# Kernel tuning notes

Hardware: AMD Instinct MI355X
Metric: run time of the kernel (lower is better)

Reference implementation:

```python
import jax, jax.numpy as jnp
import numpy as np

N = 50000      # nodes
E = 800000     # edges per relation
R = 2          # relations
L = 2          # conv layers
D = 128        # hidden / input channels
G = 64         # graphs in batch
C = 8          # num_classes


def setup_inputs() -> dict:
    key = jax.random.key(0)
    ks = jax.random.split(key, 6)
    x = jax.random.normal(ks[0], (N, D), dtype=jnp.float32)
    W = jax.random.normal(ks[1], (L, R, D, D), dtype=jnp.float32) * 0.05
    b = jnp.zeros((L, R, D), dtype=jnp.float32)
    lin_w = jax.random.normal(ks[2], (D, C), dtype=jnp.float32) * 0.05
    lin_b = jnp.zeros((C,), dtype=jnp.float32)
    edge_index = jax.random.randint(ks[3], (R, 2, E), 0, N, dtype=jnp.int32)
    batch = jnp.sort(jax.random.randint(ks[4], (N,), 0, G, dtype=jnp.int32))
    return {"x": x, "W": W, "b": b, "lin_w": lin_w, "lin_b": lin_b,
            "edge_index": edge_index, "batch": batch}


def _gcn_conv(x, src, dst, inv_sqrt_deg, W_r, b_r):
    """PyG GCNConv: symmetric-normalized aggregation with self loops.
    out[i] = sum_{j->i} d_i^-1/2 d_j^-1/2 (x_j W) + d_i^-1 (x_i W) + b
    where d includes the self loop (in-degree + 1)."""
    xw = x @ W_r                                   # [N, D]
    norm = inv_sqrt_deg[src] * inv_sqrt_deg[dst]   # [E]
    agg = jax.ops.segment_sum(xw[src] * norm[:, None], dst, num_segments=N)
    agg = agg + xw * (inv_sqrt_deg * inv_sqrt_deg)[:, None]  # self-loop msg
    return agg + b_r


def reference(x, W, b, lin_w, lin_b, edge_index, batch):
    # Pre-compute per-relation symmetric normalization (same for all layers).
    inv_sqrt_degs = []
    for r in range(R):
        dst = edge_index[r, 1]
        deg = jax.ops.segment_sum(jnp.ones((E,), x.dtype), dst, num_segments=N) + 1.0
        inv_sqrt_degs.append(jax.lax.rsqrt(deg))

    h = x
    for l in range(L):
        out = jnp.zeros((N, D), x.dtype)
        for r in range(R):  # HeteroConv aggr='sum' over relations
            out = out + _gcn_conv(h, edge_index[r, 0], edge_index[r, 1],
                                  inv_sqrt_degs[r], W[l, r], b[l, r])
        h = jax.nn.relu(out) if l < L - 1 else out

    # global_mean_pool over batch ids
    counts = jax.ops.segment_sum(jnp.ones((N,), x.dtype), batch, num_segments=G)
    sums = jax.ops.segment_sum(h, batch, num_segments=G)
    pooled = sums / jnp.maximum(counts, 1.0)[:, None]   # [G, D]
    # dropout(p=0.5) is identity in eval mode; final Linear
    return pooled @ lin_w + lin_b                        # [G, C]
```

## Files before the change

kernel.cpp:

```cpp
#include <hip/hip_runtime.h>
#include <math.h>

#define NN 50000
#define EE 800000
#define RR 2
#define LL 2
#define DD 128
#define GG 64
#define CCLS 8
#define NBUK 196
#define BCAP 6144
#define BCI  7424

typedef unsigned int uint;
typedef unsigned short ushort;
typedef short bf16x8 __attribute__((ext_vector_type(8)));
typedef float f32x4 __attribute__((ext_vector_type(4)));
typedef float f32x2 __attribute__((ext_vector_type(2)));

#define OFF_H1    ((size_t)0)
#define OFF_WBT   ((size_t)12800000)
#define OFF_ISD   ((size_t)12931072)
#define OFF_RP    ((size_t)13331072)
#define OFF_CI    ((size_t)14131072)
#define OFF_ZERO  ((size_t)25771904)
#define OFF_BD    ((size_t)25806592)
#define OFF_XW    ((size_t)25806592)
#define ZO_GCUR 0
#define ZO_SUM  1600
#define ZO_CNT  34368
#define ZERO_BYTES 34624

static __device__ __forceinline__ ushort f2b(float f) {
  uint u = __float_as_uint(f);
  uint r = (u + 0x7fffu + ((u >> 16) & 1u)) >> 16;
  return (ushort)r;
}
static __device__ __forceinline__ float blo(uint u) { return __uint_as_float(u << 16); }
static __device__ __forceinline__ float bhi(uint u) { return __uint_as_float(u & 0xffff0000u); }

__global__ __launch_bounds__(256) void k_wprep(const float* __restrict__ W,
                                               ushort* __restrict__ WT) {
  int idx = blockIdx.x * 256 + threadIdx.x;
  int lr = idx >> 14;
  int rem = idx & 16383;
  int n = rem >> 7, k = rem & 127;
  WT[lr * 16384 + n * 128 + k] = f2b(W[lr * 16384 + k * 128 + n]);
}

__global__ __launch_bounds__(256) void k_part(const int* __restrict__ EI,
                                              int* __restrict__ gcur,
                                              uint* __restrict__ bdata) {
  __shared__ int hist[256];
  __shared__ int sbase[256];
  __shared__ int gbase[256];
  __shared__ int lcur[256];
  __shared__ uint stage[4096];
  __shared__ unsigned char bstage[4096];
  const int r = blockIdx.y;
  const int t = threadIdx.x;
  const int e0 = blockIdx.x * 4096;
  const int cnt = min(4096, EE - e0);
  hist[t] = 0;
  lcur[t] = 0;
  __syncthreads();

  int src[16], dst[16];
  bool val[4];
#pragma unroll
  for (int j = 0; j < 4; ++j) {
    int i4 = (j * 256 + t) * 4;
    val[j] = (i4 < cnt);
    if (val[j]) {
      int4 s4 = *(const int4*)(EI + (size_t)r * 2 * EE + e0 + i4);
      int4 d4 = *(const int4*)(EI + (size_t)r * 2 * EE + EE + e0 + i4);
      src[j * 4 + 0] = s4.x; src[j * 4 + 1] = s4.y; src[j * 4 + 2] = s4.z; src[j * 4 + 3] = s4.w;
      dst[j * 4 + 0] = d4.x; dst[j * 4 + 1] = d4.y; dst[j * 4 + 2] = d4.z; dst[j * 4 + 3] = d4.w;
#pragma unroll
      for (int i = 0; i < 4; ++i) atomicAdd(&hist[dst[j * 4 + i] >> 8], 1);
    }
  }
  __syncthreads();
  int hv = hist[t];
  if (t < NBUK && hv > 0)
    gbase[t] = atomicAdd(&gcur[r * NBUK + t], hv);
  else
    gbase[t] = 0;
  sbase[t] = hv;
  __syncthreads();
  for (int off = 1; off < 256; off <<= 1) {
    int u = (t >= off) ? sbase[t - off] : 0;
    __syncthreads();
    sbase[t] += u;
    __syncthreads();
  }
  int incl = sbase[t];
  hist[t] = incl - hv;
  __syncthreads();
#pragma unroll
  for (int j = 0; j < 4; ++j) {
    if (val[j]) {
#pragma unroll
      for (int i = 0; i < 4; ++i) {
        int d = dst[j * 4 + i];
        int b = d >> 8;
        int p = atomicAdd(&lcur[b], 1);
        int pos = hist[b] + p;
        stage[pos] = ((uint)src[j * 4 + i] << 8) | (uint)(d & 255);
        bstage[pos] = (unsigned char)b;
      }
    }
  }
  __syncthreads();
  for (int s = t; s < cnt; s += 256) {
    int b = (int)bstage[s];
    bdata[(size_t)(r * NBUK + b) * BCAP + gbase[b] + (s - hist[b])] = stage[s];
  }
}

__global__ __launch_bounds__(256) void k_csr(const uint* __restrict__ bdata,
                                             const int* __restrict__ gcur,
                                             float* __restrict__ isd,
                                             int* __restrict__ rps,
                                             int* __restrict__ rpc,
                                             int* __restrict__ ci) {
  __shared__ int lcnt[256];
  __shared__ int lrp[256];
  __shared__ int lcur[256];
  __shared__ int cstage[BCI];
  __shared__ int shtot;
  const int b = blockIdx.x;
  const int r = blockIdx.y;
  const int t = threadIdx.x;
  const int cnt = gcur[r * NBUK + b];
  const uint* bd = bdata + (size_t)(r * NBUK + b) * BCAP;
  lcnt[t] = 0;
  lcur[t] = 0;
  __syncthreads();
  for (int s = t; s < cnt; s += 256) atomicAdd(&lcnt[bd[s] & 255u], 1);
  __syncthreads();
  const int deg = lcnt[t];
  const int node = b * 256 + t;
  const int valid = (node < NN) ? 1 : 0;
  const int deg3 = valid ? ((deg + 1 + 3) & ~3) : 0;
  lrp[t] = deg3;
  __syncthreads();
  for (int off = 1; off < 256; off <<= 1) {
    int u = (t >= off) ? lrp[t - off] : 0;
    __syncthreads();
    lrp[t] += u;
    __syncthreads();
  }
  int incl = lrp[t];
  if (t == 255) shtot = incl;
  __syncthreads();
  lrp[t] = incl - deg3;
  __syncthreads();
  const int ex = lrp[t];
  if (valid) {
    isd[r * NN + node] = rsqrtf((float)(deg + 1));
    rps[r * NN + node] = b * BCI + ex;
    rpc[r * NN + node] = deg3;
    cstage[ex + deg] = node;
    for (int p = deg + 1; p < deg3; ++p) cstage[ex + p] = NN;
  }
  const int btot = shtot;
  if (t < 16) cstage[btot + t] = NN;
  __syncthreads();
  for (int s = t; s < cnt; s += 256) {
    uint pr = bd[s];
    int j = (int)(pr & 255u);
    int p = atomicAdd(&lcur[j], 1);
    cstage[lrp[j] + p] = (int)(pr >> 8);
  }
  __syncthreads();
  const int on = btot + 16;
  int* co = ci + (size_t)r * (NBUK * BCI) + (size_t)b * BCI;
  for (int s = t; s < on; s += 256) co[s] = cstage[s];
}

#define AL_S 72
#define WT_S 136
template <int IN_BF16>
__global__ __launch_bounds__(256) void k_gemm(const void* __restrict__ Xv,
                                              const ushort* __restrict__ WTg,
                                              const float* __restrict__ isd,
                                              uint* __restrict__ Y) {
  __shared__ ushort WTl[128 * WT_S];
  __shared__ ushort Al[128 * AL_S];
  const int r = blockIdx.y;
  const int m0b = blockIdx.x * 128;
  const int t = threadIdx.x;
  const int w = t >> 6, L = t & 63, q = L >> 4, ln = L & 15;
  uint* Yr = Y + (size_t)r * (NN + 1) * 32;
  const ushort* WTr = WTg + (size_t)r * 16384;

#pragma unroll
  for (int i = 0; i < 8; ++i) {
    int g = t + i * 256;
    int n = g >> 4, k0 = (g & 15) * 8;
    *(uint4*)(&WTl[n * WT_S + k0]) = *(const uint4*)(WTr + n * 128 + k0);
  }

  f32x4 acc[2][8];
#pragma unroll
  for (int mt = 0; mt < 2; ++mt)
#pragma unroll
    for (int nt = 0; nt < 8; ++nt) {
      acc[mt][nt][0] = 0.f; acc[mt][nt][1] = 0.f;
      acc[mt][nt][2] = 0.f; acc[mt][nt][3] = 0.f;
    }

  for (int hh = 0; hh < 2; ++hh) {
    __syncthreads();
    {
      int row = t >> 1, ch = t & 1;
      int gm = m0b + row;
      ushort* dst = &Al[row * AL_S + ch * 32];
      if (gm < NN) {
        if (IN_BF16) {
          const uint4* xp = (const uint4*)((const ushort*)Xv + (size_t)gm * 128 + hh * 64 + ch * 32);
#pragma unroll
          for (int j = 0; j < 4; ++j) ((uint4*)dst)[j] = xp[j];
        } else {
          const float4* xp = (const float4*)((const float*)Xv + (size_t)gm * 128 + hh * 64 + ch * 32);
          ushort tmp[32];
#pragma unroll
          for (int j = 0; j < 8; ++j) {
            float4 v = xp[j];
            tmp[j * 4 + 0] = f2b(v.x); tmp[j * 4 + 1] = f2b(v.y);
            tmp[j * 4 + 2] = f2b(v.z); tmp[j * 4 + 3] = f2b(v.w);
          }
#pragma unroll
          for (int j = 0; j < 4; ++j) ((uint4*)dst)[j] = ((uint4*)tmp)[j];
        }
      } else {
        uint4 z = make_uint4(0, 0, 0, 0);
#pragma unroll
        for (int j = 0; j < 4; ++j) ((uint4*)dst)[j] = z;
      }
    }
    __syncthreads();
#pragma unroll
    for (int kk = 0; kk < 2; ++kk) {
      bf16x8 b0 = *(const bf16x8*)(&Al[(w * 32 + ln) * AL_S + kk * 32 + q * 8]);
      bf16x8 b1 = *(const bf16x8*)(&Al[(w * 32 + 16 + ln) * AL_S + kk * 32 + q * 8]);
#pragma unroll
      for (int nt = 0; nt < 8; ++nt) {
        bf16x8 a = *(const bf16x8*)(&WTl[(nt * 16 + ln) * WT_S + hh * 64 + kk * 32 + q * 8]);
        acc[0][nt] = __builtin_amdgcn_mfma_f32_16x16x32_bf16(a, b0, acc[0][nt], 0, 0, 0);
        acc[1][nt] = __builtin_amdgcn_mfma_f32_16x16x32_bf16(a, b1, acc[1][nt], 0, 0, 0);
      }
    }
  }
#pragma unroll
  for (int mt = 0; mt < 2; ++mt) {
    int m = m0b + w * 32 + mt * 16 + ln;
    if (m <= NN) {
      float sc = (m < NN) ? isd[r * NN + m] : 0.f;
      uint* yp = Yr + (size_t)m * 32;
#pragma unroll
      for (int nt = 0; nt < 8; ++nt) {
        f32x4 v = acc[mt][nt];
        uint u = __builtin_amdgcn_cvt_pk_fp8_f32(v[0] * sc, v[1] * sc, 0u, false);
        u = __builtin_amdgcn_cvt_pk_fp8_f32(v[2] * sc, v[3] * sc, u, true);
        yp[nt * 4 + q] = u;
      }
    }
  }
}

__global__ __launch_bounds__(256) void k_agg(const char* __restrict__ xw,
                                             const int* __restrict__ rps,
                                             const int* __restrict__ rpc,
                                             const int* __restrict__ ci,
                                             const float* __restrict__ isd,
                                             const float* __restrict__ bias,
                                             uint* __restrict__ hout, int relu_flag) {
  const int w = threadIdx.x >> 6;
  const int lane = threadIdx.x & 63;
  const int g = lane >> 4, c = lane & 15;
  const int i = blockIdx.x * 4 + w;
  const uint cb = (uint)c * 8u;

  f32x2 tot[4];
#pragma unroll
  for (int j = 0; j < 4; ++j) { tot[j][0] = 0.f; tot[j][1] = 0.f; }

#pragma unroll
  for (int r = 0; r < RR; ++r) {
    const char* xwr = xw + (size_t)r * ((size_t)(NN + 1) * 128);
    const int e0 = rps[r * NN + i];
    const int total = rpc[r * NN + i];
    const int* ce = ci + (size_t)r * (NBUK * BCI) + e0;
    const float di = isd[r * NN + i];

    f32x2 acc[4];
#pragma unroll
    for (int j = 0; j < 4; ++j) { acc[j][0] = 0.f; acc[j][1] = 0.f; }

    int s0 = ce[g];
    uint2 ucur = *(const uint2*)(xwr + (((uint)s0 << 7) + cb));
    int s1 = ce[4 + g];
    int ip = 8 + g;
    for (int base = 0; base < total; base += 4) {
      uint2 unext = *(const uint2*)(xwr + (((uint)s1 << 7) + cb));
      int s2 = ce[ip];
      ip += 4;
      f32x2 v;
      v = __builtin_amdgcn_cvt_pk_f32_fp8(ucur.x, false); acc[0] += v;
      v = __builtin_amdgcn_cvt_pk_f32_fp8(ucur.x, true);  acc[1] += v;
      v = __builtin_amdgcn_cvt_pk_f32_fp8(ucur.y, false); acc[2] += v;
      v = __builtin_amdgcn_cvt_pk_f32_fp8(ucur.y, true);  acc[3] += v;
      ucur = unext;
      s1 = s2;
    }
    f32x2 d2; d2[0] = di; d2[1] = di;
#pragma unroll
    for (int j = 0; j < 4; ++j) tot[j] += acc[j] * d2;
  }

#pragma unroll
  for (int mask = 16; mask <= 32; mask <<= 1) {
#pragma unroll
    for (int j = 0; j < 4; ++j) {
      f32x2 o;
      o[0] = __shfl_xor(tot[j][0], mask);
      o[1] = __shfl_xor(tot[j][1], mask);
      tot[j] += o;
    }
  }

  if (g == 0) {
    const int ch0 = c * 8;
    const float4* b0p = (const float4*)(bias + ch0);
    const float4* b1p = (const float4*)(bias + DD + ch0);
    float4 ba = b0p[0], bb = b0p[1], bc = b1p[0], bd = b1p[1];
    float o[8] = {tot[0][0], tot[0][1], tot[1][0], tot[1][1],
                  tot[2][0], tot[2][1], tot[3][0], tot[3][1]};
    o[0] += ba.x + bc.x; o[1] += ba.y + bc.y; o[2] += ba.z + bc.z; o[3] += ba.w + bc.w;
    o[4] += bb.x + bd.x; o[5] += bb.y + bd.y; o[6] += bb.z + bd.z; o[7] += bb.w + bd.w;
    if (relu_flag) {
#pragma unroll
      for (int j = 0; j < 8; ++j) o[j] = fmaxf(o[j], 0.f);
    }
    uint4 pk;
    pk.x = (uint)f2b(o[0]) | ((uint)f2b(o[1]) << 16);
    pk.y = (uint)f2b(o[2]) | ((uint)f2b(o[3]) << 16);
    pk.z = (uint)f2b(o[4]) | ((uint)f2b(o[5]) << 16);
    pk.w = (uint)f2b(o[6]) | ((uint)f2b(o[7]) << 16);
    ((uint4*)(hout + (size_t)i * 64))[c] = pk;
  }
}

#define PCHUNK 32
__global__ __launch_bounds__(64) void k_pool(const uint* __restrict__ h,
                                             const int* __restrict__ batch,
                                             float* __restrict__ sums,
                                             int* __restrict__ counts) {
  int lane = threadIdx.x;
  int n0 = blockIdx.x * PCHUNK;
  int n1 = n0 + PCHUNK;
  if (n1 > NN) n1 = NN;
  if (n0 >= NN) return;
  float aLo = 0.f, aHi = 0.f;
  int cnt = 0;
  int g = batch[n0];
  uint u = h[(size_t)n0 * 64 + lane];
  for (int n = n0; n < n1; ++n) {
    uint unext = 0;
    int gnext = g;
    if (n + 1 < n1) {
      unext = h[(size_t)(n + 1) * 64 + lane];
      gnext = batch[n + 1];
    }
    aLo += blo(u);
    aHi += bhi(u);
    cnt++;
    if (n + 1 < n1 && gnext != g) {
      atomicAdd(&sums[g * DD + lane * 2], aLo);
      atomicAdd(&sums[g * DD + lane * 2 + 1], aHi);
      if (lane == 0) atomicAdd(&counts[g], cnt);
      aLo = 0.f; aHi = 0.f; cnt = 0;
      g = gnext;
    }
    u = unext;
  }
  atomicAdd(&sums[g * DD + lane * 2], aLo);
  atomicAdd(&sums[g * DD + lane * 2 + 1], aHi);
  if (lane == 0) atomicAdd(&counts[g], cnt);
}

__global__ __launch_bounds__(512) void k_final(const float* __restrict__ sums,
                                               const int* __restrict__ counts,
                                               const float* __restrict__ lin_w,
                                               const float* __restrict__ lin_b,
                                               float* __restrict__ out) {
  int t = threadIdx.x;
  int g = t >> 3, co = t & 7;
  float cnt = (float)counts[g];
  if (cnt < 1.f) cnt = 1.f;
  float inv = 1.f / cnt;
  float v = lin_b[co];
  for (int d = 0; d < DD; ++d) v += (sums[g * DD + d] * inv) * lin_w[d * CCLS + co];
  out[t] = v;
}

extern "C" void kernel_launch(void* const* d_in, const int* in_sizes, int n_in,
                              void* d_out, int out_size, void* d_ws, size_t ws_size,
                              hipStream_t stream) {
  (void)in_sizes; (void)n_in; (void)out_size; (void)ws_size;
  const float* x     = (const float*)d_in[0];
  const float* W     = (const float*)d_in[1];
  const float* b     = (const float*)d_in[2];
  const float* lin_w = (const float*)d_in[3];
  const float* lin_b = (const float*)d_in[4];
  const int*   EI    = (const int*)d_in[5];
  const int*   batch = (const int*)d_in[6];
  float* out = (float*)d_out;

  char* ws = (char*)d_ws;
  uint*   h1    = (uint*)(ws + OFF_H1);
  ushort* WbfT  = (ushort*)(ws + OFF_WBT);
  float*  isd   = (float*)(ws + OFF_ISD);
  int*    rps   = (int*)(ws + OFF_RP);
  int*    rpc   = rps + 2 * NN;
  int*    ci    = (int*)(ws + OFF_CI);
  uint*   bdata = (uint*)(ws + OFF_BD);
  uint*   xw    = (uint*)(ws + OFF_XW);
  char*   zb    = ws + OFF_ZERO;
  int*    gcur  = (int*)(zb + ZO_GCUR);
  float*  sums  = (float*)(zb + ZO_SUM);
  int*    counts= (int*)(zb + ZO_CNT);

  (void)hipMemsetAsync(zb, 0, ZERO_BYTES, stream);

  k_wprep<<<256, 256, 0, stream>>>(W, WbfT);
  k_part<<<dim3((EE + 4095) / 4096, RR), 256, 0, stream>>>(EI, gcur, bdata);
  k_csr<<<dim3(NBUK, RR), 256, 0, stream>>>(bdata, gcur, isd, rps, rpc, ci);

  for (int l = 0; l < LL; ++l) {
    const ushort* WTl_g = WbfT + (size_t)l * RR * DD * DD;
    if (l == 0)
      k_gemm<0><<<dim3((NN + 127) / 128, RR), 256, 0, stream>>>((const void*)x, WTl_g, isd, xw);
    else
      k_gemm<1><<<dim3((NN + 127) / 128, RR), 256, 0, stream>>>((const void*)h1, WTl_g, isd, xw);
    k_agg<<<(NN + 3) / 4, 256, 0, stream>>>((const char*)xw, rps, rpc, ci, isd,
                                            b + (size_t)l * RR * DD, h1,
                                            (l < LL - 1) ? 1 : 0);
  }
  k_pool<<<(NN + PCHUNK - 1) / PCHUNK, 64, 0, stream>>>(h1, batch, sums, counts);
  k_final<<<1, GG * CCLS, 0, stream>>>(sums, counts, lin_w, lin_b, out);
}
```

Measured before the change: 289.3 us.

## Merge both relations into one CSR and process four nodes per wave in aggregation

The CSR build now runs one block per bucket for both relations together. It interleaves each node's neighbour lists for relation 0 and relation 1 into a single contiguous index stream, padded to groups of 8, with relation-1 indices offset into the second xw slab. The aggregation kernel assigns four consecutive nodes to each wave, uses 8 edge groups with 16-byte loads per lane, and keeps a continuous software pipeline across relations and nodes to hide gather latency and cut per-node setup. Padding to 8 adds wasted gathers for low-degree nodes, and the row-pointer layout and workspace offsets change.

```diff
diff --git a/kernel.cpp b/kernel.cpp
--- a/kernel.cpp
+++ b/kernel.cpp
@@ -10,7 +10,7 @@
 #define CCLS 8
 #define NBUK 196
 #define BCAP 6144
-#define BCI  7424
+#define BCI2 14080
 
 typedef unsigned int uint;
 typedef unsigned short ushort;
@@ -22,10 +22,10 @@
 #define OFF_WBT   ((size_t)12800000)
 #define OFF_ISD   ((size_t)12931072)
 #define OFF_RP    ((size_t)13331072)
-#define OFF_CI    ((size_t)14131072)
-#define OFF_ZERO  ((size_t)25771904)
-#define OFF_BD    ((size_t)25806592)
-#define OFF_XW    ((size_t)25806592)
+#define OFF_CI    ((size_t)13732480)
+#define OFF_ZERO  ((size_t)24771200)
+#define OFF_BD    ((size_t)24805824)
+#define OFF_XW    ((size_t)24805824)
 #define ZO_GCUR 0
 #define ZO_SUM  1600
 #define ZO_CNT  34368
@@ -124,26 +124,29 @@
                                              int* __restrict__ rps,
                                              int* __restrict__ rpc,
                                              int* __restrict__ ci) {
-  __shared__ int lcnt[256];
-  __shared__ int lrp[256];
-  __shared__ int lcur[256];
-  __shared__ int cstage[BCI];
+  __shared__ int lcnt0[256], lcnt1[256], lrp[256], lex[256], lng[256];
+  __shared__ int lcurA[256], lcurB[256];
+  __shared__ int cstage[BCI2];
   __shared__ int shtot;
   const int b = blockIdx.x;
-  const int r = blockIdx.y;
   const int t = threadIdx.x;
-  const int cnt = gcur[r * NBUK + b];
-  const uint* bd = bdata + (size_t)(r * NBUK + b) * BCAP;
-  lcnt[t] = 0;
-  lcur[t] = 0;
-  __syncthreads();
-  for (int s = t; s < cnt; s += 256) atomicAdd(&lcnt[bd[s] & 255u], 1);
-  __syncthreads();
-  const int deg = lcnt[t];
+  const int cnt0 = gcur[b];
+  const int cnt1 = gcur[NBUK + b];
+  const uint* bd0 = bdata + (size_t)b * BCAP;
+  const uint* bd1 = bdata + (size_t)(NBUK + b) * BCAP;
+  lcnt0[t] = 0; lcnt1[t] = 0; lcurA[t] = 0; lcurB[t] = 0;
+  __syncthreads();
+  for (int s = t; s < cnt0; s += 256) atomicAdd(&lcnt0[bd0[s] & 255u], 1);
+  for (int s = t; s < cnt1; s += 256) atomicAdd(&lcnt1[bd1[s] & 255u], 1);
+  __syncthreads();
+  const int deg0 = lcnt0[t];
+  const int deg1 = lcnt1[t];
   const int node = b * 256 + t;
   const int valid = (node < NN) ? 1 : 0;
-  const int deg3 = valid ? ((deg + 1 + 3) & ~3) : 0;
-  lrp[t] = deg3;
+  const int ng0 = valid ? ((deg0 + 8) >> 3) : 0;
+  const int ng1 = valid ? ((deg1 + 8) >> 3) : 0;
+  const int sz = (ng0 + ng1) << 3;
+  lrp[t] = sz;
   __syncthreads();
   for (int off = 1; off < 256; off <<= 1) {
     int u = (t >= off) ? lrp[t - off] : 0;
@@ -151,31 +154,40 @@
     lrp[t] += u;
     __syncthreads();
   }
-  int incl = lrp[t];
+  const int incl = lrp[t];
   if (t == 255) shtot = incl;
-  __syncthreads();
-  lrp[t] = incl - deg3;
-  __syncthreads();
-  const int ex = lrp[t];
+  const int ex = incl - sz;
+  lex[t] = ex;
+  lng[t] = ng0;
+  __syncthreads();
+  const int btot = shtot;
+  if (t < 32) cstage[btot + t] = NN;
+  rps[node] = b * BCI2 + ex;
+  rpc[node] = ng0 | (ng1 << 16);
   if (valid) {
-    isd[r * NN + node] = rsqrtf((float)(deg + 1));
-    rps[r * NN + node] = b * BCI + ex;
-    rpc[r * NN + node] = deg3;
-    cstage[ex + deg] = node;
-    for (int p = deg + 1; p < deg3; ++p) cstage[ex + p] = NN;
-  }
-  const int btot = shtot;
-  if (t < 16) cstage[btot + t] = NN;
-  __syncthreads();
-  for (int s = t; s < cnt; s += 256) {
-    uint pr = bd[s];
+    isd[node] = rsqrtf((float)(deg0 + 1));
+    isd[NN + node] = rsqrtf((float)(deg1 + 1));
+    cstage[ex + deg0] = node;
+    for (int p = deg0 + 1; p < (ng0 << 3); ++p) cstage[ex + p] = NN;
+    const int ex1 = ex + (ng0 << 3);
+    cstage[ex1 + deg1] = (NN + 1) + node;
+    for (int p = deg1 + 1; p < (ng1 << 3); ++p) cstage[ex1 + p] = NN;
+  }
+  for (int s = t; s < cnt0; s += 256) {
+    uint pr = bd0[s];
     int j = (int)(pr & 255u);
-    int p = atomicAdd(&lcur[j], 1);
-    cstage[lrp[j] + p] = (int)(pr >> 8);
-  }
-  __syncthreads();
-  const int on = btot + 16;
-  int* co = ci + (size_t)r * (NBUK * BCI) + (size_t)b * BCI;
+    int p = atomicAdd(&lcurA[j], 1);
+    cstage[lex[j] + p] = (int)(pr >> 8);
+  }
+  for (int s = t; s < cnt1; s += 256) {
+    uint pr = bd1[s];
+    int j = (int)(pr & 255u);
+    int p = atomicAdd(&lcurB[j], 1);
+    cstage[lex[j] + (lng[j] << 3) + p] = (int)(pr >> 8) + (NN + 1);
+  }
+  __syncthreads();
+  const int on = btot + 32;
+  int* co = ci + (size_t)b * BCI2;
   for (int s = t; s < on; s += 256) co[s] = cstage[s];
 }
 
@@ -270,6 +282,22 @@
   }
 }
 
+#define AGG_STEP()                                                           \
+  {                                                                          \
+    int s3 = ce0[ip]; ip += 8;                                               \
+    uint4 u2 = *(const uint4*)(xw + ((size_t)((uint)s2 << 7) + cb));         \
+    f32x2 v;                                                                 \
+    v = __builtin_amdgcn_cvt_pk_f32_fp8(u0.x, false); acc[0] += v;           \
+    v = __builtin_amdgcn_cvt_pk_f32_fp8(u0.x, true);  acc[1] += v;           \
+    v = __builtin_amdgcn_cvt_pk_f32_fp8(u0.y, false); acc[2] += v;           \
+    v = __builtin_amdgcn_cvt_pk_f32_fp8(u0.y, true);  acc[3] += v;           \
+    v = __builtin_amdgcn_cvt_pk_f32_fp8(u0.z, false); acc[4] += v;           \
+    v = __builtin_amdgcn_cvt_pk_f32_fp8(u0.z, true);  acc[5] += v;           \
+    v = __builtin_amdgcn_cvt_pk_f32_fp8(u0.w, false); acc[6] += v;           \
+    v = __builtin_amdgcn_cvt_pk_f32_fp8(u0.w, true);  acc[7] += v;           \
+    u0 = u1; u1 = u2; s2 = s3;                                               \
+  }
+
 __global__ __launch_bounds__(256) void k_agg(const char* __restrict__ xw,
                                              const int* __restrict__ rps,
                                              const int* __restrict__ rpc,
@@ -279,77 +307,82 @@
                                              uint* __restrict__ hout, int relu_flag) {
   const int w = threadIdx.x >> 6;
   const int lane = threadIdx.x & 63;
-  const int g = lane >> 4, c = lane & 15;
-  const int i = blockIdx.x * 4 + w;
-  const uint cb = (uint)c * 8u;
-
-  f32x2 tot[4];
-#pragma unroll
-  for (int j = 0; j < 4; ++j) { tot[j][0] = 0.f; tot[j][1] = 0.f; }
-
-#pragma unroll
-  for (int r = 0; r < RR; ++r) {
-    const char* xwr = xw + (size_t)r * ((size_t)(NN + 1) * 128);
-    const int e0 = rps[r * NN + i];
-    const int total = rpc[r * NN + i];
-    const int* ce = ci + (size_t)r * (NBUK * BCI) + e0;
-    const float di = isd[r * NN + i];
-
-    f32x2 acc[4];
-#pragma unroll
-    for (int j = 0; j < 4; ++j) { acc[j][0] = 0.f; acc[j][1] = 0.f; }
-
-    int s0 = ce[g];
-    uint2 ucur = *(const uint2*)(xwr + (((uint)s0 << 7) + cb));
-    int s1 = ce[4 + g];
-    int ip = 8 + g;
-    for (int base = 0; base < total; base += 4) {
-      uint2 unext = *(const uint2*)(xwr + (((uint)s1 << 7) + cb));
-      int s2 = ce[ip];
-      ip += 4;
-      f32x2 v;
-      v = __builtin_amdgcn_cvt_pk_f32_fp8(ucur.x, false); acc[0] += v;
-      v = __builtin_amdgcn_cvt_pk_f32_fp8(ucur.x, true);  acc[1] += v;
-      v = __builtin_amdgcn_cvt_pk_f32_fp8(ucur.y, false); acc[2] += v;
-      v = __builtin_amdgcn_cvt_pk_f32_fp8(ucur.y, true);  acc[3] += v;
-      ucur = unext;
-      s1 = s2;
-    }
-    f32x2 d2; d2[0] = di; d2[1] = di;
-#pragma unroll
-    for (int j = 0; j < 4; ++j) tot[j] += acc[j] * d2;
-  }
-
-#pragma unroll
-  for (int mask = 16; mask <= 32; mask <<= 1) {
-#pragma unroll
-    for (int j = 0; j < 4; ++j) {
-      f32x2 o;
-      o[0] = __shfl_xor(tot[j][0], mask);
-      o[1] = __shfl_xor(tot[j][1], mask);
-      tot[j] += o;
-    }
-  }
-
-  if (g == 0) {
-    const int ch0 = c * 8;
-    const float4* b0p = (const float4*)(bias + ch0);
-    const float4* b1p = (const float4*)(bias + DD + ch0);
-    float4 ba = b0p[0], bb = b0p[1], bc = b1p[0], bd = b1p[1];
-    float o[8] = {tot[0][0], tot[0][1], tot[1][0], tot[1][1],
-                  tot[2][0], tot[2][1], tot[3][0], tot[3][1]};
-    o[0] += ba.x + bc.x; o[1] += ba.y + bc.y; o[2] += ba.z + bc.z; o[3] += ba.w + bc.w;
-    o[4] += bb.x + bd.x; o[5] += bb.y + bd.y; o[6] += bb.z + bd.z; o[7] += bb.w + bd.w;
-    if (relu_flag) {
-#pragma unroll
-      for (int j = 0; j < 8; ++j) o[j] = fmaxf(o[j], 0.f);
-    }
-    uint4 pk;
-    pk.x = (uint)f2b(o[0]) | ((uint)f2b(o[1]) << 16);
-    pk.y = (uint)f2b(o[2]) | ((uint)f2b(o[3]) << 16);
-    pk.z = (uint)f2b(o[4]) | ((uint)f2b(o[5]) << 16);
-    pk.w = (uint)f2b(o[6]) | ((uint)f2b(o[7]) << 16);
-    ((uint4*)(hout + (size_t)i * 64))[c] = pk;
+  const int g = lane >> 3, c = lane & 7;
+  const int wid = blockIdx.x * 4 + w;
+  const int n0 = (wid >> 6) * 256 + (wid & 63) * 4;
+  const size_t cb = (size_t)c * 16;
+
+  const int m0 = rpc[n0], m1 = rpc[n0 + 1], m2 = rpc[n0 + 2], m3 = rpc[n0 + 3];
+  const int* ce0 = ci + rps[n0];
+
+  int ip = g;
+  int s0 = ce0[ip]; ip += 8;
+  int s1 = ce0[ip]; ip += 8;
+  int s2 = ce0[ip]; ip += 8;
+  uint4 u0 = *(const uint4*)(xw + ((size_t)((uint)s0 << 7) + cb));
+  uint4 u1 = *(const uint4*)(xw + ((size_t)((uint)s1 << 7) + cb));
+
+#pragma unroll
+  for (int k = 0; k < 4; ++k) {
+    const int node = n0 + k;
+    const int meta_k = (k == 0) ? m0 : (k == 1) ? m1 : (k == 2) ? m2 : m3;
+    const int ng0 = meta_k & 0xffff;
+    const int ng1 = (meta_k >> 16) & 0xffff;
+    const float di0 = isd[node];
+    const float di1 = isd[NN + node];
+
+    f32x2 acc[8];
+#pragma unroll
+    for (int j = 0; j < 8; ++j) { acc[j][0] = 0.f; acc[j][1] = 0.f; }
+    for (int q = 0; q < ng0; ++q) AGG_STEP();
+    f32x2 t8[8];
+    {
+      f32x2 d; d[0] = di0; d[1] = di0;
+#pragma unroll
+      for (int j = 0; j < 8; ++j) { t8[j] = acc[j] * d; acc[j][0] = 0.f; acc[j][1] = 0.f; }
+    }
+    for (int q = 0; q < ng1; ++q) AGG_STEP();
+    {
+      f32x2 d; d[0] = di1; d[1] = di1;
+#pragma unroll
+      for (int j = 0; j < 8; ++j) t8[j] += acc[j] * d;
+    }
+
+#pragma unroll
+    for (int mask = 8; mask <= 32; mask <<= 1) {
+#pragma unroll
+      for (int j = 0; j < 8; ++j) {
+        f32x2 o;
+        o[0] = __shfl_xor(t8[j][0], mask);
+        o[1] = __shfl_xor(t8[j][1], mask);
+        t8[j] += o;
+      }
+    }
+
+    if (g == 0 && node < NN) {
+      const float4* p0 = (const float4*)(bias + c * 16);
+      const float4* p1 = (const float4*)(bias + DD + c * 16);
+      float o[16];
+#pragma unroll
+      for (int j = 0; j < 4; ++j) {
+        float4 a = p0[j], bq = p1[j];
+        o[4 * j + 0] = t8[2 * j][0] + a.x + bq.x;
+        o[4 * j + 1] = t8[2 * j][1] + a.y + bq.y;
+        o[4 * j + 2] = t8[2 * j + 1][0] + a.z + bq.z;
+        o[4 * j + 3] = t8[2 * j + 1][1] + a.w + bq.w;
+      }
+      if (relu_flag) {
+#pragma unroll
+        for (int j = 0; j < 16; ++j) o[j] = fmaxf(o[j], 0.f);
+      }
+      uint pk[8];
+#pragma unroll
+      for (int j = 0; j < 8; ++j)
+        pk[j] = (uint)f2b(o[2 * j]) | ((uint)f2b(o[2 * j + 1]) << 16);
+      uint4* dst = (uint4*)(hout + (size_t)node * 64) + c * 2;
+      dst[0] = make_uint4(pk[0], pk[1], pk[2], pk[3]);
+      dst[1] = make_uint4(pk[4], pk[5], pk[6], pk[7]);
+    }
   }
 }
 
@@ -424,7 +457,7 @@
   ushort* WbfT  = (ushort*)(ws + OFF_WBT);
   float*  isd   = (float*)(ws + OFF_ISD);
   int*    rps   = (int*)(ws + OFF_RP);
-  int*    rpc   = rps + 2 * NN;
+  int*    rpc   = rps + NBUK * 256;
   int*    ci    = (int*)(ws + OFF_CI);
   uint*   bdata = (uint*)(ws + OFF_BD);
   uint*   xw    = (uint*)(ws + OFF_XW);
@@ -437,7 +470,7 @@
 
   k_wprep<<<256, 256, 0, stream>>>(W, WbfT);
   k_part<<<dim3((EE + 4095) / 4096, RR), 256, 0, stream>>>(EI, gcur, bdata);
-  k_csr<<<dim3(NBUK, RR), 256, 0, stream>>>(bdata, gcur, isd, rps, rpc, ci);
+  k_csr<<<NBUK, 256, 0, stream>>>(bdata, gcur, isd, rps, rpc, ci);
 
   for (int l = 0; l < LL; ++l) {
     const ushort* WTl_g = WbfT + (size_t)l * RR * DD * DD;
@@ -445,9 +478,9 @@
       k_gemm<0><<<dim3((NN + 127) / 128, RR), 256, 0, stream>>>((const void*)x, WTl_g, isd, xw);
     else
       k_gemm<1><<<dim3((NN + 127) / 128, RR), 256, 0, stream>>>((const void*)h1, WTl_g, isd, xw);
-    k_agg<<<(NN + 3) / 4, 256, 0, stream>>>((const char*)xw, rps, rpc, ci, isd,
-                                            b + (size_t)l * RR * DD, h1,
-                                            (l < LL - 1) ? 1 : 0);
+    k_agg<<<(NBUK * 64) / 4, 256, 0, stream>>>((const char*)xw, rps, rpc, ci, isd,
+                                               b + (size_t)l * RR * DD, h1,
+                                               (l < LL - 1) ? 1 : 0);
   }
   k_pool<<<(NN + PCHUNK - 1) / PCHUNK, 64, 0, stream>>>(h1, batch, sums, counts);
   k_final<<<1, GG * CCLS, 0, stream>>>(sums, counts, lin_w, lin_b, out);
```

Result: no change. 288.1 us (-0.4%).

## Widen aggregation gather to 16-byte loads with 8 edges per wave step

Applied to the files above, without the earlier changes.

The aggregation kernel now splits each wave into 8 edge groups of 8 lanes, each lane loading 16 fp8 channels with a single uint4 load instead of 4 groups of 16 lanes loading 8 bytes. To match, the CSR build pads each node's edge list (plus self loop) to a multiple of 8 and stores a group count. The node arrays are padded to NPAD so the launch covers whole buckets, and the software prefetch of the next row is dropped. This aims for fewer, wider memory transactions per edge, at the cost of more padding entries, more accumulator registers and a longer shuffle reduction.

```diff
diff --git a/kernel.cpp b/kernel.cpp
--- a/kernel.cpp
+++ b/kernel.cpp
@@ -9,8 +9,9 @@
 #define GG 64
 #define CCLS 8
 #define NBUK 196
+#define NPAD 50176
 #define BCAP 6144
-#define BCI  7424
+#define BCI  8256
 
 typedef unsigned int uint;
 typedef unsigned short ushort;
@@ -22,10 +23,10 @@
 #define OFF_WBT   ((size_t)12800000)
 #define OFF_ISD   ((size_t)12931072)
 #define OFF_RP    ((size_t)13331072)
-#define OFF_CI    ((size_t)14131072)
-#define OFF_ZERO  ((size_t)25771904)
-#define OFF_BD    ((size_t)25806592)
-#define OFF_XW    ((size_t)25806592)
+#define OFF_CI    ((size_t)14133888)
+#define OFF_ZERO  ((size_t)27079296)
+#define OFF_BD    ((size_t)27113920)
+#define OFF_XW    ((size_t)27113920)
 #define ZO_GCUR 0
 #define ZO_SUM  1600
 #define ZO_CNT  34368
@@ -124,9 +125,7 @@
                                              int* __restrict__ rps,
                                              int* __restrict__ rpc,
                                              int* __restrict__ ci) {
-  __shared__ int lcnt[256];
-  __shared__ int lrp[256];
-  __shared__ int lcur[256];
+  __shared__ int lcnt[256], lrp[256], lex[256], lcur[256];
   __shared__ int cstage[BCI];
   __shared__ int shtot;
   const int b = blockIdx.x;
@@ -142,8 +141,9 @@
   const int deg = lcnt[t];
   const int node = b * 256 + t;
   const int valid = (node < NN) ? 1 : 0;
-  const int deg3 = valid ? ((deg + 1 + 3) & ~3) : 0;
-  lrp[t] = deg3;
+  const int ng = valid ? ((deg + 8) >> 3) : 0;
+  const int sz = ng << 3;
+  lrp[t] = sz;
   __syncthreads();
   for (int off = 1; off < 256; off <<= 1) {
     int u = (t >= off) ? lrp[t - off] : 0;
@@ -151,31 +151,29 @@
     lrp[t] += u;
     __syncthreads();
   }
-  int incl = lrp[t];
+  const int incl = lrp[t];
   if (t == 255) shtot = incl;
-  __syncthreads();
-  lrp[t] = incl - deg3;
-  __syncthreads();
-  const int ex = lrp[t];
+  lex[t] = incl - sz;
+  __syncthreads();
+  const int ex = lex[t];
+  const int btot = shtot;
+  rps[r * NPAD + node] = b * BCI + ex;
+  rpc[r * NPAD + node] = ng;
+  if (t < 16) cstage[btot + t] = NN;
   if (valid) {
     isd[r * NN + node] = rsqrtf((float)(deg + 1));
-    rps[r * NN + node] = b * BCI + ex;
-    rpc[r * NN + node] = deg3;
     cstage[ex + deg] = node;
-    for (int p = deg + 1; p < deg3; ++p) cstage[ex + p] = NN;
-  }
-  const int btot = shtot;
-  if (t < 16) cstage[btot + t] = NN;
-  __syncthreads();
+    for (int p = deg + 1; p < sz; ++p) cstage[ex + p] = NN;
+  }
   for (int s = t; s < cnt; s += 256) {
     uint pr = bd[s];
     int j = (int)(pr & 255u);
     int p = atomicAdd(&lcur[j], 1);
-    cstage[lrp[j] + p] = (int)(pr >> 8);
-  }
-  __syncthreads();
+    cstage[lex[j] + p] = (int)(pr >> 8);
+  }
+  __syncthreads();
+  int* co = ci + (size_t)(r * NBUK + b) * BCI;
   const int on = btot + 16;
-  int* co = ci + (size_t)r * (NBUK * BCI) + (size_t)b * BCI;
   for (int s = t; s < on; s += 256) co[s] = cstage[s];
 }
 
@@ -279,51 +277,52 @@
                                              uint* __restrict__ hout, int relu_flag) {
   const int w = threadIdx.x >> 6;
   const int lane = threadIdx.x & 63;
-  const int g = lane >> 4, c = lane & 15;
-  const int i = blockIdx.x * 4 + w;
-  const uint cb = (uint)c * 8u;
-
-  f32x2 tot[4];
-#pragma unroll
-  for (int j = 0; j < 4; ++j) { tot[j][0] = 0.f; tot[j][1] = 0.f; }
+  const int g = lane >> 3, c = lane & 7;
+  const int node = blockIdx.x * 4 + w;
+  const size_t cb = (size_t)c * 16;
+  const int nsafe = (node < NN) ? node : 0;
+
+  f32x2 tot[8];
+#pragma unroll
+  for (int j = 0; j < 8; ++j) { tot[j][0] = 0.f; tot[j][1] = 0.f; }
 
 #pragma unroll
   for (int r = 0; r < RR; ++r) {
     const char* xwr = xw + (size_t)r * ((size_t)(NN + 1) * 128);
-    const int e0 = rps[r * NN + i];
-    const int total = rpc[r * NN + i];
-    const int* ce = ci + (size_t)r * (NBUK * BCI) + e0;
-    const float di = isd[r * NN + i];
-
-    f32x2 acc[4];
-#pragma unroll
-    for (int j = 0; j < 4; ++j) { acc[j][0] = 0.f; acc[j][1] = 0.f; }
-
-    int s0 = ce[g];
-    uint2 ucur = *(const uint2*)(xwr + (((uint)s0 << 7) + cb));
-    int s1 = ce[4 + g];
+    const int* ce = ci + (size_t)r * (NBUK * BCI) + rps[r * NPAD + node];
+    const int ng = rpc[r * NPAD + node];
+    const float di = isd[r * NN + nsafe];
+
+    f32x2 acc[8];
+#pragma unroll
+    for (int j = 0; j < 8; ++j) { acc[j][0] = 0.f; acc[j][1] = 0.f; }
+
+    int s_cur = ce[g];
     int ip = 8 + g;
-    for (int base = 0; base < total; base += 4) {
-      uint2 unext = *(const uint2*)(xwr + (((uint)s1 << 7) + cb));
-      int s2 = ce[ip];
-      ip += 4;
+    for (int q = 0; q < ng; ++q) {
+      int s_next = ce[ip];
+      ip += 8;
+      uint4 u = *(const uint4*)(xwr + ((((size_t)(uint)s_cur) << 7) + cb));
       f32x2 v;
-      v = __builtin_amdgcn_cvt_pk_f32_fp8(ucur.x, false); acc[0] += v;
-      v = __builtin_amdgcn_cvt_pk_f32_fp8(ucur.x, true);  acc[1] += v;
-      v = __builtin_amdgcn_cvt_pk_f32_fp8(ucur.y, false); acc[2] += v;
-      v = __builtin_amdgcn_cvt_pk_f32_fp8(ucur.y, true);  acc[3] += v;
-      ucur = unext;
-      s1 = s2;
+      v = __builtin_amdgcn_cvt_pk_f32_fp8(u.x, false); acc[0] += v;
+      v = __builtin_amdgcn_cvt_pk_f32_fp8(u.x, true);  acc[1] += v;
+      v = __builtin_amdgcn_cvt_pk_f32_fp8(u.y, false); acc[2] += v;
+      v = __builtin_amdgcn_cvt_pk_f32_fp8(u.y, true);  acc[3] += v;
+      v = __builtin_amdgcn_cvt_pk_f32_fp8(u.z, false); acc[4] += v;
+      v = __builtin_amdgcn_cvt_pk_f32_fp8(u.z, true);  acc[5] += v;
+      v = __builtin_amdgcn_cvt_pk_f32_fp8(u.w, false); acc[6] += v;
+      v = __builtin_amdgcn_cvt_pk_f32_fp8(u.w, true);  acc[7] += v;
+      s_cur = s_next;
     }
     f32x2 d2; d2[0] = di; d2[1] = di;
 #pragma unroll
-    for (int j = 0; j < 4; ++j) tot[j] += acc[j] * d2;
-  }
-
-#pragma unroll
-  for (int mask = 16; mask <= 32; mask <<= 1) {
-#pragma unroll
-    for (int j = 0; j < 4; ++j) {
+    for (int j = 0; j < 8; ++j) tot[j] += acc[j] * d2;
+  }
+
+#pragma unroll
+  for (int mask = 8; mask <= 32; mask <<= 1) {
+#pragma unroll
+    for (int j = 0; j < 8; ++j) {
       f32x2 o;
       o[0] = __shfl_xor(tot[j][0], mask);
       o[1] = __shfl_xor(tot[j][1], mask);
@@ -331,25 +330,29 @@
     }
   }
 
-  if (g == 0) {
-    const int ch0 = c * 8;
-    const float4* b0p = (const float4*)(bias + ch0);
-    const float4* b1p = (const float4*)(bias + DD + ch0);
-    float4 ba = b0p[0], bb = b0p[1], bc = b1p[0], bd = b1p[1];
-    float o[8] = {tot[0][0], tot[0][1], tot[1][0], tot[1][1],
-                  tot[2][0], tot[2][1], tot[3][0], tot[3][1]};
-    o[0] += ba.x + bc.x; o[1] += ba.y + bc.y; o[2] += ba.z + bc.z; o[3] += ba.w + bc.w;
-    o[4] += bb.x + bd.x; o[5] += bb.y + bd.y; o[6] += bb.z + bd.z; o[7] += bb.w + bd.w;
+  if (g == 0 && node < NN) {
+    const float4* p0 = (const float4*)(bias + c * 16);
+    const float4* p1 = (const float4*)(bias + DD + c * 16);
+    float o[16];
+#pragma unroll
+    for (int j = 0; j < 4; ++j) {
+      float4 a = p0[j], bq = p1[j];
+      o[4 * j + 0] = tot[2 * j][0] + a.x + bq.x;
+      o[4 * j + 1] = tot[2 * j][1] + a.y + bq.y;
+      o[4 * j + 2] = tot[2 * j + 1][0] + a.z + bq.z;
+      o[4 * j + 3] = tot[2 * j + 1][1] + a.w + bq.w;
+    }
     if (relu_flag) {
 #pragma unroll
-      for (int j = 0; j < 8; ++j) o[j] = fmaxf(o[j], 0.f);
-    }
-    uint4 pk;
-    pk.x = (uint)f2b(o[0]) | ((uint)f2b(o[1]) << 16);
-    pk.y = (uint)f2b(o[2]) | ((uint)f2b(o[3]) << 16);
-    pk.z = (uint)f2b(o[4]) | ((uint)f2b(o[5]) << 16);
-    pk.w = (uint)f2b(o[6]) | ((uint)f2b(o[7]) << 16);
-    ((uint4*)(hout + (size_t)i * 64))[c] = pk;
+      for (int j = 0; j < 16; ++j) o[j] = fmaxf(o[j], 0.f);
+    }
+    uint pk[8];
+#pragma unroll
+    for (int j = 0; j < 8; ++j)
+      pk[j] = (uint)f2b(o[2 * j]) | ((uint)f2b(o[2 * j + 1]) << 16);
+    uint4* dst = (uint4*)(hout + (size_t)node * 64) + c * 2;
+    dst[0] = make_uint4(pk[0], pk[1], pk[2], pk[3]);
+    dst[1] = make_uint4(pk[4], pk[5], pk[6], pk[7]);
   }
 }
 
@@ -424,7 +427,7 @@
   ushort* WbfT  = (ushort*)(ws + OFF_WBT);
   float*  isd   = (float*)(ws + OFF_ISD);
   int*    rps   = (int*)(ws + OFF_RP);
-  int*    rpc   = rps + 2 * NN;
+  int*    rpc   = rps + 2 * NPAD;
   int*    ci    = (int*)(ws + OFF_CI);
   uint*   bdata = (uint*)(ws + OFF_BD);
   uint*   xw    = (uint*)(ws + OFF_XW);
@@ -445,9 +448,9 @@
       k_gemm<0><<<dim3((NN + 127) / 128, RR), 256, 0, stream>>>((const void*)x, WTl_g, isd, xw);
     else
       k_gemm<1><<<dim3((NN + 127) / 128, RR), 256, 0, stream>>>((const void*)h1, WTl_g, isd, xw);
-    k_agg<<<(NN + 3) / 4, 256, 0, stream>>>((const char*)xw, rps, rpc, ci, isd,
-                                            b + (size_t)l * RR * DD, h1,
-                                            (l < LL - 1) ? 1 : 0);
+    k_agg<<<NPAD / 4, 256, 0, stream>>>((const char*)xw, rps, rpc, ci, isd,
+                                        b + (size_t)l * RR * DD, h1,
+                                        (l < LL - 1) ? 1 : 0);
   }
   k_pool<<<(NN + PCHUNK - 1) / PCHUNK, 64, 0, stream>>>(h1, batch, sums, counts);
   k_final<<<1, GG * CCLS, 0, stream>>>(sums, counts, lin_w, lin_b, out);
```

New measurement: 287.5 us. Within noise of the previous version (-0.6%).
